# Kernel tuning notes

Hardware: AMD Instinct MI355X
Metric: run time of the kernel (lower is better)

Reference implementation:

```python
import jax, jax.numpy as jnp
import numpy as np
import math

D_MODEL = 1024
N_HEADS = 16
D_HEAD = D_MODEL // N_HEADS
B, T = 2, 2048


def setup_inputs() -> dict:
    key = jax.random.key(0)
    ks = jax.random.split(key, 5)
    x = jax.random.normal(ks[0], (B, T, D_MODEL), dtype=jnp.float32)
    W_qkv = jax.random.normal(ks[1], (D_MODEL, 3 * D_MODEL), dtype=jnp.float32) * 0.02
    b_qkv = jnp.zeros((3 * D_MODEL,), dtype=jnp.float32)
    W_g = jax.random.normal(ks[2], (N_HEADS, D_HEAD, D_HEAD), dtype=jnp.float32) * 0.02
    W_out = jax.random.normal(ks[3], (D_MODEL, D_MODEL), dtype=jnp.float32) * 0.02
    b_out = jnp.zeros((D_MODEL,), dtype=jnp.float32)
    return {"x": x, "W_qkv": W_qkv, "b_qkv": b_qkv, "W_g": W_g, "W_out": W_out, "b_out": b_out}


def reference(x, W_qkv, b_qkv, W_g, W_out, b_out):
    b, t, d = x.shape
    h, dh = N_HEADS, D_HEAD
    qkv = x @ W_qkv + b_qkv                         # (B,T,3D)
    q, k, v = jnp.split(qkv, 3, axis=-1)
    # (B,T,D) -> (B,H,T,dh)
    q = q.reshape(b, t, h, dh).transpose(0, 2, 1, 3)
    k = k.reshape(b, t, h, dh).transpose(0, 2, 1, 3)
    v = v.reshape(b, t, h, dh).transpose(0, 2, 1, 3)
    scale = 1.0 / math.sqrt(dh)
    scores = jnp.einsum('bhtd,bhsd->bhts', q, k) * scale   # (B,H,T,T)
    causal = jnp.tril(jnp.ones((t, t), dtype=bool))
    scores = jnp.where(causal, scores, jnp.float32(-jnp.inf))
    attn = jax.nn.softmax(scores, axis=-1)
    # query-conditioned bilinear value gate (applied at each position)
    g = jax.nn.sigmoid(jnp.einsum('bhtd,hde->bhte', q, W_g))  # (B,H,T,dh)
    v = g * v
    out = jnp.einsum('bhts,bhsd->bhtd', attn, v)             # (B,H,T,dh)
    out = out.transpose(0, 2, 1, 3).reshape(b, t, d)
    return out @ W_out + b_out
```

## Files before the change

### kernel.cpp

```cpp
#include <hip/hip_runtime.h>
#include <hip/hip_bf16.h>

typedef unsigned short ushortT;
typedef __bf16 bf16x8 __attribute__((ext_vector_type(8)));
typedef float f32x4 __attribute__((ext_vector_type(4)));
typedef float f32x16 __attribute__((ext_vector_type(16)));

#define T_SEQ 2048
#define DH 64
#define NH 16
#define DM 1024
#define TD 3072
#define BATCH 2
#define LOG2E 1.44269504f

#define BARRIER()   asm volatile("s_barrier" ::: "memory")
#define VMCNT(n)    asm volatile("s_waitcnt vmcnt(" #n ")" ::: "memory")

__device__ inline ushortT f2bf(float f){
    union { float f; unsigned int u; } a; a.f = f;
    unsigned int r = a.u + 0x7fffu + ((a.u >> 16) & 1u);
    return (ushortT)(r >> 16);
}
__device__ inline float bf2f(ushortT u){
    union { float f; unsigned int u; } a; a.u = ((unsigned int)u) << 16;
    return a.f;
}

__device__ inline void gload_lds16(const void* g, void* l){
    __builtin_amdgcn_global_load_lds((const __attribute__((address_space(1))) void*)g,
                                     (__attribute__((address_space(3))) void*)l, 16, 0, 0);
}

__global__ __launch_bounds__(256) void prep_kernel(const float* __restrict__ x,
                                                   ushortT* __restrict__ xbf,
                                                   const float* __restrict__ Wqkv,
                                                   ushortT* __restrict__ wqkvT,
                                                   const float* __restrict__ Wout,
                                                   ushortT* __restrict__ woutT,
                                                   const float* __restrict__ Wg,
                                                   ushortT* __restrict__ wgT){
    __shared__ float tile[64][65];
    int blk = blockIdx.x, tid = threadIdx.x;
    if (blk < 4096){
        int i = (blk * 256 + tid) * 4;
        float4 v = *(const float4*)&x[i];
        xbf[i+0] = f2bf(v.x); xbf[i+1] = f2bf(v.y);
        xbf[i+2] = f2bf(v.z); xbf[i+3] = f2bf(v.w);
        return;
    }
    int c = tid & 63, r4 = tid >> 6;
    if (blk >= 5120){
        int h = blk - 5120;
#pragma unroll
        for (int i = 0; i < 16; i++){
            int d = r4 + i*4;
            tile[d][c] = Wg[h*4096 + d*64 + c];
        }
        __syncthreads();
#pragma unroll
        for (int i = 0; i < 16; i++){
            int e = r4 + i*4;
            wgT[h*4096 + e*64 + c] = f2bf(tile[c][e]);
        }
        return;
    }
    const float* in; ushortT* out; int K, N, n0, k0;
    if (blk < 4864){
        int t = blk - 4096; in = Wqkv; out = wqkvT; K = 1024; N = 3072;
        n0 = (t % 48) * 64; k0 = (t / 48) * 64;
    } else {
        int t = blk - 4864; in = Wout; out = woutT; K = 1024; N = 1024;
        n0 = (t & 15) * 64; k0 = (t >> 4) * 64;
    }
#pragma unroll
    for (int i = 0; i < 16; i++){
        int k = r4 + i * 4;
        tile[k][c] = in[(size_t)(k0 + k) * N + n0 + c];
    }
    __syncthreads();
#pragma unroll
    for (int i = 0; i < 16; i++){
        int n = r4 + i * 4;
        out[(size_t)(n0 + n) * K + k0 + c] = f2bf(tile[c][n]);
    }
}

__global__ __launch_bounds__(256) void gemm_bf16_kernel(const ushortT* __restrict__ A,
                                                        const ushortT* __restrict__ BT,
                                                        const float* __restrict__ bias,
                                                        ushortT* __restrict__ C,
                                                        int M, int N, int K){
    __shared__ __align__(16) ushortT As[2][128*32];
    __shared__ __align__(16) ushortT Bs[2][128*32];
    int tid = threadIdx.x;
    int m0 = blockIdx.x * 128;
    int n0 = blockIdx.y * 128;
    int wid = tid >> 6, lane = tid & 63;
    int l15 = lane & 15, g = lane >> 4;
    int wr = wid >> 1, wc = wid & 1;

    f32x4 acc[4][4];
#pragma unroll
    for (int i = 0; i < 4; i++)
#pragma unroll
        for (int j = 0; j < 4; j++) acc[i][j] = (f32x4){0.f,0.f,0.f,0.f};

    int srow = wid * 32 + (lane >> 2);
    int sch  = lane & 3;

#define GSTAGE(buf, k0)                                                                  \
    {                                                                                    \
        _Pragma("unroll")                                                                \
        for (int i_ = 0; i_ < 2; i_++){                                                  \
            int row_ = srow + i_ * 16;                                                   \
            const ushortT* asrc_ = A  + (size_t)(m0 + row_) * K + (k0) + sch * 8;        \
            const ushortT* bsrc_ = BT + (size_t)(n0 + row_) * K + (k0) + sch * 8;        \
            gload_lds16(asrc_, (char*)As[buf] + (wid*2 + i_) * 1024);                    \
            gload_lds16(bsrc_, (char*)Bs[buf] + (wid*2 + i_) * 1024);                    \
        }                                                                                \
    }

    GSTAGE(0, 0);

    int nk = K >> 5;
    for (int kt = 0; kt < nk; kt++){
        int buf = kt & 1;
        BARRIER();
        if (kt + 1 < nk){
            GSTAGE(buf ^ 1, (kt + 1) * 32);
            VMCNT(4);
        } else {
            VMCNT(0);
        }
        BARRIER();

        bf16x8 af[4], bfr[4];
#pragma unroll
        for (int mi = 0; mi < 4; mi++){
            int r = wr*64 + mi*16 + l15;
            af[mi]  = *(const bf16x8*)(As[buf] + r*32 + g*8);
        }
#pragma unroll
        for (int ni = 0; ni < 4; ni++){
            int r = wc*64 + ni*16 + l15;
            bfr[ni] = *(const bf16x8*)(Bs[buf] + r*32 + g*8);
        }
#pragma unroll
        for (int mi = 0; mi < 4; mi++)
#pragma unroll
            for (int ni = 0; ni < 4; ni++)
                acc[mi][ni] = __builtin_amdgcn_mfma_f32_16x16x32_bf16(af[mi], bfr[ni], acc[mi][ni], 0, 0, 0);
    }
#undef GSTAGE

#pragma unroll
    for (int mi = 0; mi < 4; mi++){
#pragma unroll
        for (int jj = 0; jj < 4; jj++){
            int mm = m0 + wr*64 + mi*16 + 4*g + jj;
#pragma unroll
            for (int ni = 0; ni < 4; ni++){
                int nn = n0 + wc*64 + ni*16 + l15;
                C[(size_t)mm * N + nn] = f2bf(acc[mi][ni][jj] + bias[nn]);
            }
        }
    }
}

__global__ __launch_bounds__(256) void gemm_out_kernel(const ushortT* __restrict__ A,
                                                       const ushortT* __restrict__ BT,
                                                       const float* __restrict__ bias,
                                                       float* __restrict__ C,
                                                       int M, int N, int K){
    __shared__ __align__(16) ushortT As[2][64*32];
    __shared__ __align__(16) ushortT Bs[2][128*32];
    int tid = threadIdx.x;
    int m0 = blockIdx.x * 64;
    int n0 = blockIdx.y * 128;
    int wid = tid >> 6, lane = tid & 63;
    int l15 = lane & 15, g = lane >> 4;
    int wr = wid >> 1, wc = wid & 1;

    f32x4 acc[2][4];
#pragma unroll
    for (int i = 0; i < 2; i++)
#pragma unroll
        for (int j = 0; j < 4; j++) acc[i][j] = (f32x4){0.f,0.f,0.f,0.f};

    int srow = tid >> 2;
    int sch  = tid & 3;

#define GSTAGE(buf, k0)                                                                  \
    {                                                                                    \
        gload_lds16(A + (size_t)(m0 + srow) * K + (k0) + sch * 8,                        \
                    (char*)As[buf] + tid * 16);                                          \
        _Pragma("unroll")                                                                \
        for (int i_ = 0; i_ < 2; i_++){                                                  \
            int row_ = srow + i_ * 64;                                                   \
            gload_lds16(BT + (size_t)(n0 + row_) * K + (k0) + sch * 8,                   \
                        (char*)Bs[buf] + (i_*256 + tid) * 16);                           \
        }                                                                                \
    }

    GSTAGE(0, 0);

    int nk = K >> 5;
    for (int kt = 0; kt < nk; kt++){
        int buf = kt & 1;
        BARRIER();
        if (kt + 1 < nk){
            GSTAGE(buf ^ 1, (kt + 1) * 32);
            VMCNT(3);
        } else {
            VMCNT(0);
        }
        BARRIER();

        bf16x8 af[2], bfr[4];
#pragma unroll
        for (int mi = 0; mi < 2; mi++){
            int r = wr*32 + mi*16 + l15;
            af[mi]  = *(const bf16x8*)(As[buf] + r*32 + g*8);
        }
#pragma unroll
        for (int ni = 0; ni < 4; ni++){
            int r = wc*64 + ni*16 + l15;
            bfr[ni] = *(const bf16x8*)(Bs[buf] + r*32 + g*8);
        }
#pragma unroll
        for (int mi = 0; mi < 2; mi++)
#pragma unroll
            for (int ni = 0; ni < 4; ni++)
                acc[mi][ni] = __builtin_amdgcn_mfma_f32_16x16x32_bf16(af[mi], bfr[ni], acc[mi][ni], 0, 0, 0);
    }
#undef GSTAGE

#pragma unroll
    for (int mi = 0; mi < 2; mi++){
#pragma unroll
        for (int jj = 0; jj < 4; jj++){
            int mm = m0 + wr*32 + mi*16 + 4*g + jj;
#pragma unroll
            for (int ni = 0; ni < 4; ni++){
                int nn = n0 + wc*64 + ni*16 + l15;
                C[(size_t)mm * N + nn] = acc[mi][ni][jj] + bias[nn];
            }
        }
    }
}

__global__ __launch_bounds__(256) void gate_kernel(const ushortT* __restrict__ qkv,
                                                   const ushortT* __restrict__ WgT,
                                                   ushortT* __restrict__ vgT){
    __shared__ __align__(16) ushortT VT[64][72];
    int tblk = blockIdx.x, bh = blockIdx.y;
    int b = bh >> 4, h = bh & 15;
    int tid = threadIdx.x, wid = tid >> 6, lane = tid & 63;
    int l15 = lane & 15, g = lane >> 4;
    int t0 = tblk * 64;
    int tl = wid*16 + l15;

    const ushortT* qrow = qkv + ((size_t)b*T_SEQ + t0 + tl)*TD + h*DH;
    bf16x8 qf0 = *(const bf16x8*)(qrow + 8*g);
    bf16x8 qf1 = *(const bf16x8*)(qrow + 32 + 8*g);

    const ushortT* wbase = WgT + h*4096;
    const ushortT* vrow = qkv + ((size_t)b*T_SEQ + t0 + tl)*TD + 2*DM + h*DH;

#pragma unroll
    for (int ns = 0; ns < 4; ns++){
        int e = ns*16 + l15;
        bf16x8 wf0 = *(const bf16x8*)(wbase + e*64 + 8*g);
        bf16x8 wf1 = *(const bf16x8*)(wbase + e*64 + 32 + 8*g);
        f32x4 z = (f32x4){0.f,0.f,0.f,0.f};
        z = __builtin_amdgcn_mfma_f32_16x16x32_bf16(wf0, qf0, z, 0, 0, 0);
        z = __builtin_amdgcn_mfma_f32_16x16x32_bf16(wf1, qf1, z, 0, 0, 0);
        union { ushortT u[4]; uint2 v; } v4;
        v4.v = *(const uint2*)(vrow + ns*16 + 4*g);
#pragma unroll
        for (int jj = 0; jj < 4; jj++){
            float ex = __builtin_amdgcn_exp2f(-z[jj] * LOG2E);
            float gv = __builtin_amdgcn_rcpf(1.f + ex);
            VT[ns*16 + 4*g + jj][tl] = f2bf(gv * bf2f(v4.u[jj]));
        }
    }
    __syncthreads();
    for (int i = tid; i < 64*8; i += 256){
        int e = i >> 3, c8 = (i & 7) * 8;
        *(uint4*)&vgT[((size_t)bh * DH + e) * T_SEQ + t0 + c8] = *(const uint4*)&VT[e][c8];
    }
}

struct QS32 {
    bf16x8 qf[4];
    float m_, lsum;
    f32x16 acc[2];
};

__device__ __forceinline__ void proc32(const ushortT* __restrict__ K0,
                                       const ushortT* __restrict__ V0,
                                       const ushortT* __restrict__ K1,
                                       const ushortT* __restrict__ V1,
                                       QS32& S, int t0, int t1, int myp,
                                       int qrel, int q32, int hi){
    int x7 = q32 & 7;
    bool diag0 = (t0 == myp);
    bool inv1  = (t1 > myp);
    bool diag1 = (t1 == myp);

    f32x16 s[2][2];
    __builtin_amdgcn_s_setprio(1);
#pragma unroll
    for (int T = 0; T < 2; T++){
        if (T == 1 && inv1) break;
        const ushortT* Kb = T ? K1 : K0;
#pragma unroll
        for (int h2 = 0; h2 < 2; h2++){
            f32x16 z;
#pragma unroll
            for (int i = 0; i < 16; i++) z[i] = 0.f;
#pragma unroll
            for (int c = 0; c < 4; c++){
                bf16x8 kf = *(const bf16x8*)(Kb + (32*h2 + q32)*64 + (((2*c + hi) ^ x7) * 8));
                z = __builtin_amdgcn_mfma_f32_32x32x16_bf16(kf, S.qf[c], z, 0, 0, 0);
            }
            s[T][h2] = z;
        }
    }
    __builtin_amdgcn_s_setprio(0);

    if (diag0){
#pragma unroll
        for (int h2 = 0; h2 < 2; h2++)
#pragma unroll
            for (int r = 0; r < 16; r++){
                int klog = 32*h2 + 16*(r>>3) + 4*((r>>2)&1) + (r&3);
                if (klog + 8*hi > qrel) s[0][h2][r] = -INFINITY;
            }
    }
    if (!inv1 && diag1){
#pragma unroll
        for (int h2 = 0; h2 < 2; h2++)
#pragma unroll
            for (int r = 0; r < 16; r++){
                int klog = 32*h2 + 16*(r>>3) + 4*((r>>2)&1) + (r&3);
                if (klog + 8*hi > qrel) s[1][h2][r] = -INFINITY;
            }
    }

    float tmax = -INFINITY;
#pragma unroll
    for (int T = 0; T < 2; T++){
        if (T == 1 && inv1) break;
#pragma unroll
        for (int h2 = 0; h2 < 2; h2++)
#pragma unroll
            for (int r = 0; r < 16; r++) tmax = fmaxf(tmax, s[T][h2][r]);
    }
    tmax = fmaxf(tmax, __shfl_xor(tmax, 32, 64));

    float mnew = fmaxf(S.m_, tmax);
    float mc = mnew * LOG2E;
    if (!__all(mnew == S.m_)){
        float alpha = __builtin_amdgcn_exp2f(fmaf(S.m_, LOG2E, -mc));
#pragma unroll
        for (int eh = 0; eh < 2; eh++)
#pragma unroll
            for (int i = 0; i < 16; i++) S.acc[eh][i] *= alpha;
        S.lsum *= alpha;
        S.m_ = mnew;
    }

    float rs = 0.f;
    __builtin_amdgcn_s_setprio(1);
#pragma unroll
    for (int T = 0; T < 2; T++){
        if (T == 1 && inv1) break;
        const ushortT* Vb = T ? V1 : V0;
#pragma unroll
        for (int ck = 0; ck < 4; ck++){
            bf16x8 pa;
            int h2 = ck >> 1;
#pragma unroll
            for (int j = 0; j < 8; j++){
                int r = 8*(ck & 1) + 4*(j >> 2) + (j & 3);
                float p = __builtin_amdgcn_exp2f(fmaf(s[T][h2][r], LOG2E, -mc));
                rs += p;
                pa[j] = (__bf16)p;
            }
#pragma unroll
            for (int eh = 0; eh < 2; eh++){
                bf16x8 vf = *(const bf16x8*)(Vb + (32*eh + q32)*64 + (((2*ck + hi) ^ x7) * 8));
                S.acc[eh] = __builtin_amdgcn_mfma_f32_32x32x16_bf16(vf, pa, S.acc[eh], 0, 0, 0);
            }
        }
    }
    __builtin_amdgcn_s_setprio(0);

    rs += __shfl_xor(rs, 32, 64);
    S.lsum += rs;
}

__global__ __launch_bounds__(256, 2) void attn_kernel(const ushortT* __restrict__ qkv,
                                                      const ushortT* __restrict__ vgT,
                                                      ushortT* __restrict__ obf){
    __shared__ __align__(16) ushortT Ks[2][2][64*64];
    __shared__ __align__(16) ushortT Vs[2][2][64*64];
    int bh = blockIdx.x, y = blockIdx.y;
    int pairid = (y < 8) ? y : 23 - y;
    int b = bh >> 4, h = bh & 15;
    int tid = threadIdx.x, wid = tid >> 6, lane = tid & 63;
    int q32 = lane & 31, hi = lane >> 5;
    int grp = wid >> 1;
    int qh  = wid & 1;

    const ushortT* Kg = qkv + (size_t)b * T_SEQ * TD + DM + h * DH;
    const ushortT* Vg = vgT + (size_t)bh * DH * T_SEQ;

    int pA = pairid, pB = 31 - pairid;
    int myp = grp ? pB : pA;
    int qrel = qh*32 + q32;

    int sr  = tid >> 3;
    int sc8 = tid & 7;

#define STAGE_ROUND(buf, rr)                                                             \
    {                                                                                    \
        int t0_ = 2*(rr);     if (t0_ > pB) t0_ = pB;                                    \
        int t1_ = 2*(rr) + 1; if (t1_ > pB) t1_ = pB;                                    \
        _Pragma("unroll")                                                                \
        for (int i_ = 0; i_ < 2; i_++){                                                  \
            int row_ = sr + 32*i_;                                                       \
            int sc_  = sc8 ^ (row_ & 7);                                                 \
            int r32_ = row_ & 31;                                                        \
            int pr_  = 32*i_ + ((r32_ & ~12) | ((r32_ & 4) << 1) | ((r32_ & 8) >> 1));   \
            gload_lds16(Kg + (size_t)(t0_*64 + pr_) * TD + sc_*8,                        \
                        (char*)Ks[buf][0] + tid*16 + i_*4096);                           \
            gload_lds16(Kg + (size_t)(t1_*64 + pr_) * TD + sc_*8,                        \
                        (char*)Ks[buf][1] + tid*16 + i_*4096);                           \
            gload_lds16(Vg + (size_t)row_ * T_SEQ + t0_*64 + sc_*8,                      \
                        (char*)Vs[buf][0] + tid*16 + i_*4096);                           \
            gload_lds16(Vg + (size_t)row_ * T_SEQ + t1_*64 + sc_*8,                      \
                        (char*)Vs[buf][1] + tid*16 + i_*4096);                           \
        }                                                                                \
    }

    QS32 S;
    {
        int qrow = myp*64 + qrel;
        const ushortT* qb = qkv + ((size_t)b * T_SEQ + qrow) * TD + h * DH + 8*hi;
#pragma unroll
        for (int c = 0; c < 4; c++){
            S.qf[c] = *(const bf16x8*)(qb + 16*c);
#pragma unroll
            for (int j = 0; j < 8; j++)
                S.qf[c][j] = (__bf16)((float)S.qf[c][j] * 0.125f);
        }
        S.m_ = -INFINITY; S.lsum = 0.f;
#pragma unroll
        for (int eh = 0; eh < 2; eh++)
#pragma unroll
            for (int i = 0; i < 16; i++) S.acc[eh][i] = 0.f;
    }

    int nr = (33 - pairid) >> 1;
    STAGE_ROUND(0, 0);

    for (int r = 0; r < nr; r++){
        int buf = r & 1;
        BARRIER();
        if (r + 1 < nr){
            STAGE_ROUND(buf ^ 1, r + 1);
            VMCNT(8);
        } else {
            VMCNT(0);
        }
        BARRIER();
        int t0 = 2*r;
        if (t0 <= myp)
            proc32(Ks[buf][0], Vs[buf][0], Ks[buf][1], Vs[buf][1],
                   S, t0, t0 + 1, myp, qrel, q32, hi);
    }
#undef STAGE_ROUND

    float inv = 1.f / S.lsum;
    size_t orow = ((size_t)b * T_SEQ + myp*64 + qrel) * DM + h*DH;
#pragma unroll
    for (int eh = 0; eh < 2; eh++){
#pragma unroll
        for (int a = 0; a < 4; a++){
            union { ushortT u[4]; uint2 v; } pk;
#pragma unroll
            for (int bb = 0; bb < 4; bb++)
                pk.u[bb] = f2bf(S.acc[eh][4*a + bb] * inv);
            *(uint2*)&obf[orow + 32*eh + 8*a + 4*hi] = pk.v;
        }
    }
}

extern "C" void kernel_launch(void* const* d_in, const int* in_sizes, int n_in,
                              void* d_out, int out_size, void* d_ws, size_t ws_size,
                              hipStream_t stream){
    const float* x    = (const float*)d_in[0];
    const float* Wqkv = (const float*)d_in[1];
    const float* bqkv = (const float*)d_in[2];
    const float* Wg   = (const float*)d_in[3];
    const float* Wout = (const float*)d_in[4];
    const float* bout = (const float*)d_in[5];

    char* ws = (char*)d_ws;
    ushortT* xbf   = (ushortT*)(ws);
    ushortT* wqkvT = (ushortT*)(ws + 8388608);
    ushortT* woutT = (ushortT*)(ws + 14680064);
    ushortT* qkvb  = (ushortT*)(ws + 16777216);
    ushortT* vgT   = (ushortT*)(ws + 41943040);
    ushortT* obf   = (ushortT*)(ws + 50331648);
    ushortT* wgT   = (ushortT*)(ws + 58720256);

    prep_kernel<<<5136, 256, 0, stream>>>(x, xbf, Wqkv, wqkvT, Wout, woutT, Wg, wgT);
    gemm_bf16_kernel<<<dim3(32,24), 256, 0, stream>>>(xbf, wqkvT, bqkv, qkvb, 4096, 3072, 1024);
    gate_kernel<<<dim3(32,32), 256, 0, stream>>>(qkvb, wgT, vgT);
    attn_kernel<<<dim3(32,16), 256, 0, stream>>>(qkvb, vgT, obf);
    gemm_out_kernel<<<dim3(64,8), 256, 0, stream>>>(obf, woutT, bout, (float*)d_out, 4096, 1024, 1024);
}
```

Baseline: 114.1 us.

## Share K/V tiles across four query blocks per 512-thread attention block

Each attention workgroup grows from 256 to 512 threads and now covers four query blocks (p, 15-p, 16+p, 31-p) instead of a balanced pair. Every block therefore streams the full K/V sequence once, spread over more waves. The LDS layout of K/V is also changed to a fragment-linear order, so each lane reads its MFMA operand at lane*8 with no XOR swizzle, and the P-fragment row index is simplified to match. The aim is to halve the number of K/V loads per query and simplify LDS addressing. The cost is one block per CU, fixed 16 rounds for every block, and possible LDS bank conflicts from the unswizzled layout.

```diff
diff --git a/kernel.cpp b/kernel.cpp
--- a/kernel.cpp
+++ b/kernel.cpp
@@ -303,11 +303,11 @@
                                        const ushortT* __restrict__ K1,
                                        const ushortT* __restrict__ V1,
                                        QS32& S, int t0, int t1, int myp,
-                                       int qrel, int q32, int hi){
-    int x7 = q32 & 7;
+                                       int qrel, int lane){
     bool diag0 = (t0 == myp);
     bool inv1  = (t1 > myp);
     bool diag1 = (t1 == myp);
+    int hi = lane >> 5;
 
     f32x16 s[2][2];
     __builtin_amdgcn_s_setprio(1);
@@ -322,7 +322,7 @@
             for (int i = 0; i < 16; i++) z[i] = 0.f;
 #pragma unroll
             for (int c = 0; c < 4; c++){
-                bf16x8 kf = *(const bf16x8*)(Kb + (32*h2 + q32)*64 + (((2*c + hi) ^ x7) * 8));
+                bf16x8 kf = *(const bf16x8*)(Kb + (h2*4 + c)*512 + lane*8);
                 z = __builtin_amdgcn_mfma_f32_32x32x16_bf16(kf, S.qf[c], z, 0, 0, 0);
             }
             s[T][h2] = z;
@@ -384,14 +384,14 @@
             int h2 = ck >> 1;
 #pragma unroll
             for (int j = 0; j < 8; j++){
-                int r = 8*(ck & 1) + 4*(j >> 2) + (j & 3);
+                int r = 8*(ck & 1) + j;
                 float p = __builtin_amdgcn_exp2f(fmaf(s[T][h2][r], LOG2E, -mc));
                 rs += p;
                 pa[j] = (__bf16)p;
             }
 #pragma unroll
             for (int eh = 0; eh < 2; eh++){
-                bf16x8 vf = *(const bf16x8*)(Vb + (32*eh + q32)*64 + (((2*ck + hi) ^ x7) * 8));
+                bf16x8 vf = *(const bf16x8*)(Vb + (eh*4 + ck)*512 + lane*8);
                 S.acc[eh] = __builtin_amdgcn_mfma_f32_32x32x16_bf16(vf, pa, S.acc[eh], 0, 0, 0);
             }
         }
@@ -402,48 +402,39 @@
     S.lsum += rs;
 }
 
-__global__ __launch_bounds__(256, 2) void attn_kernel(const ushortT* __restrict__ qkv,
+__global__ __launch_bounds__(512, 1) void attn_kernel(const ushortT* __restrict__ qkv,
                                                       const ushortT* __restrict__ vgT,
                                                       ushortT* __restrict__ obf){
     __shared__ __align__(16) ushortT Ks[2][2][64*64];
     __shared__ __align__(16) ushortT Vs[2][2][64*64];
-    int bh = blockIdx.x, y = blockIdx.y;
-    int pairid = (y < 8) ? y : 23 - y;
+    int bh = blockIdx.x, p = blockIdx.y;
     int b = bh >> 4, h = bh & 15;
     int tid = threadIdx.x, wid = tid >> 6, lane = tid & 63;
     int q32 = lane & 31, hi = lane >> 5;
-    int grp = wid >> 1;
     int qh  = wid & 1;
+
+    int qbs[4] = { p, 15 - p, 16 + p, 31 - p };
+    int myp = qbs[wid >> 1];
+    int qrel = qh*32 + q32;
 
     const ushortT* Kg = qkv + (size_t)b * T_SEQ * TD + DM + h * DH;
     const ushortT* Vg = vgT + (size_t)bh * DH * T_SEQ;
 
-    int pA = pairid, pB = 31 - pairid;
-    int myp = grp ? pB : pA;
-    int qrel = qh*32 + q32;
-
-    int sr  = tid >> 3;
-    int sc8 = tid & 7;
+    int h2c = tid >> 6, lane6 = tid & 63;
+    int q32s = lane6 & 31, his = lane6 >> 5;
+    int prs  = (q32s & ~12) | ((q32s & 4) << 1) | ((q32s & 8) >> 1);
+    int kRow = 32*(h2c >> 2) + prs;
+    int kCol = (h2c & 3)*16 + 8*his;
+    int vE   = 32*(h2c >> 2) + q32s;
+    int vT   = (h2c & 3)*16 + 8*his;
 
 #define STAGE_ROUND(buf, rr)                                                             \
     {                                                                                    \
-        int t0_ = 2*(rr);     if (t0_ > pB) t0_ = pB;                                    \
-        int t1_ = 2*(rr) + 1; if (t1_ > pB) t1_ = pB;                                    \
-        _Pragma("unroll")                                                                \
-        for (int i_ = 0; i_ < 2; i_++){                                                  \
-            int row_ = sr + 32*i_;                                                       \
-            int sc_  = sc8 ^ (row_ & 7);                                                 \
-            int r32_ = row_ & 31;                                                        \
-            int pr_  = 32*i_ + ((r32_ & ~12) | ((r32_ & 4) << 1) | ((r32_ & 8) >> 1));   \
-            gload_lds16(Kg + (size_t)(t0_*64 + pr_) * TD + sc_*8,                        \
-                        (char*)Ks[buf][0] + tid*16 + i_*4096);                           \
-            gload_lds16(Kg + (size_t)(t1_*64 + pr_) * TD + sc_*8,                        \
-                        (char*)Ks[buf][1] + tid*16 + i_*4096);                           \
-            gload_lds16(Vg + (size_t)row_ * T_SEQ + t0_*64 + sc_*8,                      \
-                        (char*)Vs[buf][0] + tid*16 + i_*4096);                           \
-            gload_lds16(Vg + (size_t)row_ * T_SEQ + t1_*64 + sc_*8,                      \
-                        (char*)Vs[buf][1] + tid*16 + i_*4096);                           \
-        }                                                                                \
+        int kv0_ = (rr)*128, kv1_ = kv0_ + 64;                                           \
+        gload_lds16(Kg + (size_t)(kv0_ + kRow) * TD + kCol, (char*)Ks[buf][0] + tid*16); \
+        gload_lds16(Kg + (size_t)(kv1_ + kRow) * TD + kCol, (char*)Ks[buf][1] + tid*16); \
+        gload_lds16(Vg + (size_t)vE * T_SEQ + kv0_ + vT,    (char*)Vs[buf][0] + tid*16); \
+        gload_lds16(Vg + (size_t)vE * T_SEQ + kv1_ + vT,    (char*)Vs[buf][1] + tid*16); \
     }
 
     QS32 S;
@@ -464,15 +455,14 @@
             for (int i = 0; i < 16; i++) S.acc[eh][i] = 0.f;
     }
 
-    int nr = (33 - pairid) >> 1;
     STAGE_ROUND(0, 0);
 
-    for (int r = 0; r < nr; r++){
+    for (int r = 0; r < 16; r++){
         int buf = r & 1;
         BARRIER();
-        if (r + 1 < nr){
+        if (r < 15){
             STAGE_ROUND(buf ^ 1, r + 1);
-            VMCNT(8);
+            VMCNT(4);
         } else {
             VMCNT(0);
         }
@@ -480,7 +470,7 @@
         int t0 = 2*r;
         if (t0 <= myp)
             proc32(Ks[buf][0], Vs[buf][0], Ks[buf][1], Vs[buf][1],
-                   S, t0, t0 + 1, myp, qrel, q32, hi);
+                   S, t0, t0 + 1, myp, qrel, lane);
     }
 #undef STAGE_ROUND
 
@@ -521,6 +511,6 @@
     prep_kernel<<<5136, 256, 0, stream>>>(x, xbf, Wqkv, wqkvT, Wout, woutT, Wg, wgT);
     gemm_bf16_kernel<<<dim3(32,24), 256, 0, stream>>>(xbf, wqkvT, bqkv, qkvb, 4096, 3072, 1024);
     gate_kernel<<<dim3(32,32), 256, 0, stream>>>(qkvb, wgT, vgT);
-    attn_kernel<<<dim3(32,16), 256, 0, stream>>>(qkvb, vgT, obf);
+    attn_kernel<<<dim3(32,8), 512, 0, stream>>>(qkvb, vgT, obf);
     gemm_out_kernel<<<dim3(64,8), 256, 0, stream>>>(obf, woutT, bout, (float*)d_out, 4096, 1024, 1024);
 }
```

New measurement: 122.0 us. +6.9%, slower.
